# Performance work log

Measured on AMD Instinct MI355X. Metric: run time of the kernel, lower is better.

The kernel has to match this reference:

```python
import jax, jax.numpy as jnp
import numpy as np
import math

D_MODEL = 1024
D_STATE = 16
D_CONV = 4
EXPAND = 2
NHEADS = 8
NGROUPS = 1
D_INNER = D_MODEL * EXPAND                      # 2048
D_SSM = D_INNER - 2 * NGROUPS * D_STATE          # 2016
HEADP = D_SSM // NHEADS                          # 252
D_IN_PROJ = 4 * D_INNER + NHEADS                 # 8200
BATCH = 2
SEQLEN = 2048
DT_MIN, DT_MAX, DT_FLOOR = 1e-3, 1e-1, 1e-4


def setup_inputs() -> dict:
    key = jax.random.key(0)
    ks = jax.random.split(key, 10)
    rn = lambda k, shape, scale: (jax.random.normal(k, shape, jnp.float32) * scale)
    # dt_bias init exactly like the torch module
    dt = jnp.exp(jax.random.uniform(ks[0], (NHEADS,)) * (math.log(DT_MAX) - math.log(DT_MIN)) + math.log(DT_MIN))
    dt = jnp.clip(dt, DT_FLOOR, None)
    dt_bias = dt + jnp.log(-jnp.expm1(-dt))
    A_log = jnp.log(jax.random.uniform(ks[1], (NHEADS,), minval=0.9, maxval=0.999))
    return {
        "u": rn(ks[2], (BATCH, SEQLEN, D_MODEL), 1.0),
        "W_in": rn(ks[3], (D_MODEL, D_IN_PROJ), 0.02),
        "conv_w": rn(ks[4], (D_INNER, D_CONV), 0.2),
        "conv_b": rn(ks[5], (D_INNER,), 0.02),
        "dt_bias": dt_bias,
        "A_log": A_log,
        "Dp": jnp.ones((NHEADS,), jnp.float32),
        "ln_g": jnp.ones((D_SSM,), jnp.float32),
        "ln_b": jnp.zeros((D_SSM,), jnp.float32),
        "gate_w": rn(ks[6], (D_SSM, D_SSM), 0.02),
        "gate_b": jnp.zeros((D_SSM,), jnp.float32),
        "W_out": rn(ks[7], (D_INNER + D_SSM, D_MODEL), 0.02),
    }


def _forward(u, W_in, conv_w, conv_b, dt_bias, A_log, Dp, ln_g, ln_b, gate_w, gate_b, W_out):
    B, L, _ = u.shape
    zxbcdt = jnp.einsum('bld,de->ble', u, W_in)  # [B,L,4*Di+H]
    z0 = zxbcdt[..., :D_INNER]
    x0 = zxbcdt[..., D_INNER:2 * D_INNER]
    # z (2*Di:3*Di) is unused in the original forward
    xBC = zxbcdt[..., 3 * D_INNER:4 * D_INNER]
    dt_raw = zxbcdt[..., 4 * D_INNER:]              # [B,L,H]
    dt = jax.nn.softplus(dt_raw + dt_bias)           # [B,L,H]
    A = -jnp.exp(A_log)                              # [H]
    # depthwise causal conv1d (kernel D_CONV) + SiLU
    xc = jnp.pad(xBC, ((0, 0), (D_CONV - 1, 0), (0, 0)))
    xBC_conv = conv_b + sum(xc[:, k:k + L, :] * conv_w[:, k] for k in range(D_CONV))
    xBC_act = jax.nn.silu(xBC_conv)                  # [B,L,Di]
    x = xBC_act[..., :D_SSM].reshape(B, L, NHEADS, HEADP)   # [B,L,H,P]
    Bm = xBC_act[..., D_SSM:D_SSM + D_STATE]         # [B,L,N] (ngroups=1)
    Cm = xBC_act[..., D_SSM + D_STATE:]              # [B,L,N]

    def step(h, inp):
        dt_t, x_t, B_t, C_t = inp                    # [b,H],[b,H,P],[b,N],[b,N]
        dA = jnp.exp(dt_t * A)                       # [b,H]
        h = dA[:, :, None, None] * h + (dt_t[:, :, None] * x_t)[..., None] * B_t[:, None, None, :]
        y_t = jnp.einsum('bhpn,bn->bhp', h, C_t) + Dp[None, :, None] * x_t
        return h, y_t

    h0 = jnp.zeros((B, NHEADS, HEADP, D_STATE), u.dtype)
    xs = (dt.transpose(1, 0, 2), x.transpose(1, 0, 2, 3), Bm.transpose(1, 0, 2), Cm.transpose(1, 0, 2))
    _, ys = jax.lax.scan(step, h0, xs)               # ys: [L,B,H,P]
    y = ys.transpose(1, 0, 2, 3).reshape(B, L, D_SSM)
    # LayerNorm over d_ssm
    mu = y.mean(-1, keepdims=True)
    var = y.var(-1, keepdims=True)
    y = (y - mu) * jax.lax.rsqrt(var + 1e-5) * ln_g + ln_b
    gate = jax.nn.sigmoid(jnp.einsum('bld,de->ble', y, gate_w) + gate_b)
    y = gate * y
    mlp_skip = jax.nn.silu(z0) * x0                  # [B,L,Di]
    return jnp.einsum('ble,ed->bld', jnp.concatenate([mlp_skip, y], axis=-1), W_out)


def reference(u, W_in, conv_w, conv_b, dt_bias, A_log, Dp, ln_g, ln_b, gate_w, gate_b, W_out):
    return _forward(u, W_in, conv_w, conv_b, dt_bias, A_log, Dp, ln_g, ln_b, gate_w, gate_b, W_out)
```

## Files before the change

### kernel.cpp

```cpp
#include <hip/hip_runtime.h>
#include <hip/hip_bf16.h>
#include <math.h>

#define ROWS   4096
#define SEQLEN 2048
#define DMODEL 1024
#define DINNER 2048
#define DSSM   2016
#define NHEADS 8
#define HEADP  252
#define NPROJ  6152
#define LDPROJ 8200
#define NCAT   4064
#define NC     16
#define LC     128
#define STATE  4032

typedef unsigned short u16;
typedef __attribute__((ext_vector_type(8))) short bf16x8;
typedef __attribute__((ext_vector_type(4))) float f32x4;

__device__ __forceinline__ float sigmoidf_(float x){ return 1.f/(1.f+__expf(-x)); }
__device__ __forceinline__ float siluf_(float x){ return x/(1.f+__expf(-x)); }
__device__ __forceinline__ u16 f2b(float f){ __hip_bfloat16 h = __float2bfloat16(f); return *reinterpret_cast<u16*>(&h); }
__device__ __forceinline__ float b2f(u16 s){ __hip_bfloat16 h; *reinterpret_cast<u16*>(&h)=s; return __bfloat162float(h); }

__device__ __forceinline__ void gload16(const u16* g, u16* l) {
  __builtin_amdgcn_global_load_lds(
      (const __attribute__((address_space(1))) void*)g,
      (__attribute__((address_space(3))) void*)l, 16, 0, 0);
}

__global__ __launch_bounds__(256)
void cvt_k(const float* __restrict__ in, u16* __restrict__ out, int n4)
{
  int i = blockIdx.x*256 + threadIdx.x;
  if (i >= n4) return;
  float4 v = ((const float4*)in)[i];
  ushort4 o; o.x=f2b(v.x); o.y=f2b(v.y); o.z=f2b(v.z); o.w=f2b(v.w);
  ((ushort4*)out)[i] = o;
}

template<int REMAP>
__global__ __launch_bounds__(256)
void transcvt_k(const float* __restrict__ W, u16* __restrict__ Wt,
                int K, int N, int ldw)
{
  __shared__ float t[32][33];
  const int n0 = blockIdx.x*32, k0 = blockIdx.y*32;
  const int li = threadIdx.x & 31, lj = threadIdx.x >> 5;
  #pragma unroll
  for (int r = 0; r < 4; r++) {
    int k = k0 + lj + r*8, n = n0 + li;
    float v = 0.f;
    if (n < N) {
      int ns = REMAP ? (n < 4096 ? n : n + 2048) : n;
      v = W[(size_t)k*ldw + ns];
    }
    t[lj + r*8][li] = v;
  }
  __syncthreads();
  #pragma unroll
  for (int r = 0; r < 4; r++) {
    int n = n0 + lj + r*8, k = k0 + li;
    Wt[(size_t)n*K + k] = f2b(t[li][lj + r*8]);
  }
}

template<int MODE>
__global__ __launch_bounds__(256)
void mgemm_k(const u16* __restrict__ A, const u16* __restrict__ Bt,
             float* __restrict__ Cf, u16* __restrict__ Cb,
             const float* __restrict__ bias,
             int M, int N, int K, int ldc)
{
  __shared__ __align__(16) u16 As[128*32];
  __shared__ __align__(16) u16 Bs[128*32];
  const int tid = threadIdx.x;
  const int lane = tid & 63, wid = tid >> 6;
  const int wr = wid >> 1, wc = wid & 1;
  const int row0 = blockIdx.y * 128, col0 = blockIdx.x * 128;
  const int lg = lane >> 4, lr = lane & 15;

  const u16* gA = A  + (size_t)(row0 + wid*32 + (lane>>2))*K + (lane&3)*8;
  const u16* gB = Bt + (size_t)(col0 + wid*32 + (lane>>2))*K + (lane&3)*8;
  u16* lA = &As[wid*32*32];
  u16* lB = &Bs[wid*32*32];

  f32x4 acc[4][4];
  #pragma unroll
  for (int m=0;m<4;m++)
    #pragma unroll
    for (int n=0;n<4;n++) acc[m][n] = (f32x4){0.f,0.f,0.f,0.f};

  for (int k0 = 0; k0 < K; k0 += 32) {
    __syncthreads();
    gload16(gA,                lA);
    gload16(gA + (size_t)16*K, lA + 16*32);
    gload16(gB,                lB);
    gload16(gB + (size_t)16*K, lB + 16*32);
    gA += 32; gB += 32;
    __syncthreads();

    bf16x8 af[4], bfr[4];
    #pragma unroll
    for (int m=0;m<4;m++) af[m]  = *(const bf16x8*)&As[(wr*64 + m*16 + lr)*32 + lg*8];
    #pragma unroll
    for (int n=0;n<4;n++) bfr[n] = *(const bf16x8*)&Bs[(wc*64 + n*16 + lr)*32 + lg*8];
    #pragma unroll
    for (int m=0;m<4;m++)
      #pragma unroll
      for (int n=0;n<4;n++)
        acc[m][n] = __builtin_amdgcn_mfma_f32_16x16x32_bf16(af[m], bfr[n], acc[m][n], 0, 0, 0);
  }

  #pragma unroll
  for (int m=0;m<4;m++) {
    #pragma unroll
    for (int n=0;n<4;n++) {
      int colb = col0 + wc*64 + n*16 + lr;
      if (colb >= N) continue;
      #pragma unroll
      for (int r=0;r<4;r++) {
        int row = row0 + wr*64 + m*16 + lg*4 + r;
        float v = acc[m][n][r];
        if (MODE == 1) {
          v = sigmoidf_(v + bias[colb]) * b2f(A[(size_t)row*K + colb]);
          Cb[(size_t)row*NCAT + 2048 + colb] = f2b(v);
        } else {
          Cf[(size_t)row*ldc + colb] = v;
        }
      }
    }
  }
}

__global__ __launch_bounds__(256)
void dt_k(const float* __restrict__ zx, const float* __restrict__ dt_bias,
          float* __restrict__ dtb)
{
  int idx = blockIdx.x*256 + threadIdx.x;
  int r = idx >> 3, hh = idx & 7;
  float v = zx[(size_t)r*NPROJ + 6144 + hh] + dt_bias[hh];
  dtb[idx] = (v > 20.f) ? v : log1pf(__expf(v));
}

__global__ __launch_bounds__(256)
void conv_silu_k(const float* __restrict__ zx, const float* __restrict__ cw,
                 const float* __restrict__ cb, float* __restrict__ actb)
{
  int idx = blockIdx.x*256 + threadIdx.x;
  int c = idx & (DINNER-1);
  int r = idx >> 11;
  int l = r & (SEQLEN-1);
  float s = cb[c];
  #pragma unroll
  for (int k = 0; k < 4; k++) {
    int ll = l - 3 + k;
    if (ll >= 0) s += zx[(size_t)(r-3+k)*NPROJ + 4096 + c] * cw[c*4 + k];
  }
  actb[idx] = siluf_(s);
}

__global__ __launch_bounds__(256)
void mlp_k(const float* __restrict__ zx, u16* __restrict__ cat)
{
  int idx = blockIdx.x*256 + threadIdx.x;
  int j = idx & (DINNER-1);
  int r = idx >> 11;
  float z = zx[(size_t)r*NPROJ + j];
  float x = zx[(size_t)r*NPROJ + 2048 + j];
  cat[(size_t)r*NCAT + j] = f2b(siluf_(z) * x);
}

#define CH 32
__global__ __launch_bounds__(256)
void scan1_k(const float* __restrict__ actb, const float* __restrict__ dtb,
             const float* __restrict__ A_log,
             float* __restrict__ hloc, float* __restrict__ Pbuf)
{
  const int blk = blockIdx.x;
  const int c = blk & (NC-1), bh = blk >> 4;
  const int hh = bh & 7, b = bh >> 3;
  const int tid = threadIdx.x;
  const float Ah = -__expf(A_log[hh]);
  float h[16];
  #pragma unroll
  for (int n = 0; n < 16; n++) h[n] = 0.f;
  float dtsum = 0.f;

  __shared__ float xs[CH][HEADP+4];
  __shared__ float bs[CH][16];
  __shared__ float dts[CH];
  const int rowbase = b*SEQLEN + c*LC;

  for (int c0 = 0; c0 < LC; c0 += CH) {
    __syncthreads();
    #pragma unroll 4
    for (int s = 0; s < CH; s++) {
      const size_t rr = (size_t)(rowbase + c0 + s) * DINNER;
      if (tid < HEADP) xs[s][tid] = actb[rr + hh*HEADP + tid];
      if (tid >= 224 && tid < 240) bs[s][tid-224] = actb[rr + DSSM + (tid-224)];
    }
    if (tid < CH) dts[tid] = dtb[(size_t)(rowbase + c0 + tid)*NHEADS + hh];
    __syncthreads();

    for (int s = 0; s < CH; s++) {
      float dtv = dts[s];
      float dA  = __expf(dtv * Ah);
      float xv  = (tid < HEADP) ? xs[s][tid] : 0.f;
      float w   = dtv * xv;
      const float4* Bp = (const float4*)&bs[s][0];
      #pragma unroll
      for (int q = 0; q < 4; q++) {
        float4 Bv = Bp[q];
        h[4*q+0] = dA*h[4*q+0] + w*Bv.x;
        h[4*q+1] = dA*h[4*q+1] + w*Bv.y;
        h[4*q+2] = dA*h[4*q+2] + w*Bv.z;
        h[4*q+3] = dA*h[4*q+3] + w*Bv.w;
      }
      dtsum += dts[s];
    }
  }
  if (tid < HEADP) {
    float4* dst = (float4*)&hloc[((size_t)bh*NC + c)*STATE + tid*16];
    dst[0] = make_float4(h[0],h[1],h[2],h[3]);
    dst[1] = make_float4(h[4],h[5],h[6],h[7]);
    dst[2] = make_float4(h[8],h[9],h[10],h[11]);
    dst[3] = make_float4(h[12],h[13],h[14],h[15]);
  }
  if (tid == 0) Pbuf[bh*NC + c] = __expf(Ah * dtsum);
}

__global__ __launch_bounds__(256)
void comb_k(const float* __restrict__ hloc, const float* __restrict__ Pbuf,
            float* __restrict__ Hinit)
{
  const int bh = blockIdx.x;
  const int tid = threadIdx.x;
  __shared__ float Ps[NC];
  if (tid < NC) Ps[tid] = Pbuf[bh*NC + tid];
  __syncthreads();
  for (int e = tid; e < STATE; e += 256) {
    float H = 0.f;
    const float* hl = &hloc[(size_t)bh*NC*STATE + e];
    float* Hi = &Hinit[(size_t)bh*NC*STATE + e];
    #pragma unroll
    for (int cc = 0; cc < NC; cc++) {
      Hi[(size_t)cc*STATE] = H;
      H = Ps[cc]*H + hl[(size_t)cc*STATE];
    }
  }
}

__global__ __launch_bounds__(256)
void scan2_k(const float* __restrict__ actb, const float* __restrict__ dtb,
             const float* __restrict__ A_log, const float* __restrict__ Dp,
             const float* __restrict__ Hinit, float* __restrict__ y)
{
  const int blk = blockIdx.x;
  const int c = blk & (NC-1), bh = blk >> 4;
  const int hh = bh & 7, b = bh >> 3;
  const int tid = threadIdx.x;
  const float Ah = -__expf(A_log[hh]);
  const float Dv = Dp[hh];
  float h[16];
  if (tid < HEADP) {
    const float4* src = (const float4*)&Hinit[((size_t)bh*NC + c)*STATE + tid*16];
    float4 a0=src[0], a1=src[1], a2=src[2], a3=src[3];
    h[0]=a0.x; h[1]=a0.y; h[2]=a0.z; h[3]=a0.w;
    h[4]=a1.x; h[5]=a1.y; h[6]=a1.z; h[7]=a1.w;
    h[8]=a2.x; h[9]=a2.y; h[10]=a2.z; h[11]=a2.w;
    h[12]=a3.x; h[13]=a3.y; h[14]=a3.z; h[15]=a3.w;
  } else {
    #pragma unroll
    for (int n = 0; n < 16; n++) h[n] = 0.f;
  }

  __shared__ float xs[CH][HEADP+4];
  __shared__ float bcs[CH][32];
  __shared__ float dts[CH];
  const int rowbase = b*SEQLEN + c*LC;

  for (int c0 = 0; c0 < LC; c0 += CH) {
    __syncthreads();
    #pragma unroll 4
    for (int s = 0; s < CH; s++) {
      const size_t rr = (size_t)(rowbase + c0 + s) * DINNER;
      if (tid < HEADP) xs[s][tid] = actb[rr + hh*HEADP + tid];
      if (tid >= 224)  bcs[s][tid-224] = actb[rr + DSSM + (tid-224)];
    }
    if (tid < CH) dts[tid] = dtb[(size_t)(rowbase + c0 + tid)*NHEADS + hh];
    __syncthreads();

    for (int s = 0; s < CH; s++) {
      float dtv = dts[s];
      float dA  = __expf(dtv * Ah);
      float xv  = (tid < HEADP) ? xs[s][tid] : 0.f;
      float w   = dtv * xv;
      float acc = Dv * xv;
      const float4* Bp = (const float4*)&bcs[s][0];
      const float4* Cp = (const float4*)&bcs[s][16];
      #pragma unroll
      for (int q = 0; q < 4; q++) {
        float4 Bv = Bp[q], Cv = Cp[q];
        h[4*q+0] = dA*h[4*q+0] + w*Bv.x; acc += h[4*q+0]*Cv.x;
        h[4*q+1] = dA*h[4*q+1] + w*Bv.y; acc += h[4*q+1]*Cv.y;
        h[4*q+2] = dA*h[4*q+2] + w*Bv.z; acc += h[4*q+2]*Cv.z;
        h[4*q+3] = dA*h[4*q+3] + w*Bv.w; acc += h[4*q+3]*Cv.w;
      }
      if (tid < HEADP)
        y[(size_t)(rowbase + c0 + s)*DSSM + hh*HEADP + tid] = acc;
    }
  }
}

__global__ __launch_bounds__(256)
void ln_k(const float* __restrict__ y, const float* __restrict__ g,
          const float* __restrict__ bta, u16* __restrict__ yb)
{
  const int r = blockIdx.x;
  const int tid = threadIdx.x;
  __shared__ float r1[4], r2[4];
  __shared__ float smu, srs;
  float s1 = 0.f, s2 = 0.f;
  for (int i = tid; i < DSSM; i += 256) {
    float v = y[(size_t)r*DSSM + i];
    s1 += v; s2 += v*v;
  }
  #pragma unroll
  for (int o = 32; o > 0; o >>= 1) { s1 += __shfl_down(s1, o, 64); s2 += __shfl_down(s2, o, 64); }
  if ((tid & 63) == 0) { r1[tid>>6] = s1; r2[tid>>6] = s2; }
  __syncthreads();
  if (tid == 0) {
    float a1 = r1[0]+r1[1]+r1[2]+r1[3];
    float a2 = r2[0]+r2[1]+r2[2]+r2[3];
    float mu = a1 / (float)DSSM;
    float var = a2 / (float)DSSM - mu*mu;
    smu = mu; srs = rsqrtf(var + 1e-5f);
  }
  __syncthreads();
  float mu = smu, rs = srs;
  for (int i = tid; i < DSSM; i += 256) {
    float v = (y[(size_t)r*DSSM + i] - mu) * rs * g[i] + bta[i];
    yb[(size_t)r*DSSM + i] = f2b(v);
  }
}

extern "C" void kernel_launch(void* const* d_in, const int* in_sizes, int n_in,
                              void* d_out, int out_size, void* d_ws, size_t ws_size,
                              hipStream_t stream)
{
  const float* u      = (const float*)d_in[0];
  const float* W_in   = (const float*)d_in[1];
  const float* conv_w = (const float*)d_in[2];
  const float* conv_b = (const float*)d_in[3];
  const float* dt_bias= (const float*)d_in[4];
  const float* A_log  = (const float*)d_in[5];
  const float* Dp     = (const float*)d_in[6];
  const float* ln_g   = (const float*)d_in[7];
  const float* ln_b   = (const float*)d_in[8];
  const float* gate_w = (const float*)d_in[9];
  const float* gate_b = (const float*)d_in[10];
  const float* W_out  = (const float*)d_in[11];
  float* out = (float*)d_out;

  float* ws   = (float*)d_ws;
  float* zx   = ws;
  float* actb = zx   + (size_t)ROWS*NPROJ;
  float* dtb  = actb + (size_t)ROWS*DINNER;
  u16* u_bf   = (u16*)(dtb + (size_t)ROWS*NHEADS);
  u16* Wint   = u_bf  + (size_t)ROWS*DMODEL;
  u16* yb_bf  = Wint  + (size_t)6272*DMODEL;
  u16* cat_bf = yb_bf + (size_t)ROWS*DSSM;
  float* yb    = zx;
  float* hloc  = zx + (size_t)ROWS*DSSM;
  float* Hinit = hloc + (size_t)16*NC*STATE;
  float* Pbuf  = Hinit + (size_t)16*NC*STATE;
  u16* gwt    = (u16*)actb;
  u16* wot    = gwt + (size_t)2048*DSSM;

  dim3 blk(256);
  cvt_k<<<dim3((ROWS*DMODEL/4 + 255)/256), blk, 0, stream>>>(u, u_bf, ROWS*DMODEL/4);
  transcvt_k<1><<<dim3(6272/32, DMODEL/32), blk, 0, stream>>>(W_in, Wint, DMODEL, NPROJ, LDPROJ);
  mgemm_k<0><<<dim3(49, 32), blk, 0, stream>>>(u_bf, Wint, zx, nullptr, nullptr,
                                               ROWS, NPROJ, DMODEL, NPROJ);
  dt_k<<<dim3(ROWS*NHEADS/256), blk, 0, stream>>>(zx, dt_bias, dtb);
  conv_silu_k<<<dim3(ROWS*DINNER/256), blk, 0, stream>>>(zx, conv_w, conv_b, actb);
  mlp_k<<<dim3(ROWS*DINNER/256), blk, 0, stream>>>(zx, cat_bf);
  scan1_k<<<dim3(16*NC), blk, 0, stream>>>(actb, dtb, A_log, hloc, Pbuf);
  comb_k<<<dim3(16), blk, 0, stream>>>(hloc, Pbuf, Hinit);
  scan2_k<<<dim3(16*NC), blk, 0, stream>>>(actb, dtb, A_log, Dp, Hinit, yb);
  ln_k<<<dim3(ROWS), blk, 0, stream>>>(yb, ln_g, ln_b, yb_bf);
  transcvt_k<0><<<dim3(2048/32, DSSM/32), blk, 0, stream>>>(gate_w, gwt, DSSM, DSSM, DSSM);
  mgemm_k<1><<<dim3(16, 32), blk, 0, stream>>>(yb_bf, gwt, nullptr, cat_bf, gate_b,
                                               ROWS, DSSM, DSSM, 0);
  transcvt_k<0><<<dim3(1024/32, NCAT/32), blk, 0, stream>>>(W_out, wot, NCAT, DMODEL, DMODEL);
  mgemm_k<2><<<dim3(8, 32), blk, 0, stream>>>(cat_bf, wot, out, nullptr, nullptr,
                                              ROWS, DMODEL, NCAT, DMODEL);
}
```

Baseline: 705.0 us.

## Double-buffer GEMM LDS tiles and split scan into more, shorter chunks

The bf16 MFMA GEMM now keeps two LDS buffers per operand. It issues the global-to-LDS loads for the next K-tile before computing the current one, with one barrier per iteration instead of two, so memory latency can overlap with MFMA work. Separately, the chunked selective scan goes from 16 chunks of 128 steps to 64 chunks of 32 steps. This gives scan1/scan2 four times as many blocks for parallelism. The cost is a longer sequential combine pass in comb_k and four times the chunk-state memory traffic, plus doubled LDS use in the GEMM, which may reduce occupancy.

```diff
diff --git a/kernel.cpp b/kernel.cpp
--- a/kernel.cpp
+++ b/kernel.cpp
@@ -12,8 +12,8 @@
 #define NPROJ  6152
 #define LDPROJ 8200
 #define NCAT   4064
-#define NC     16
-#define LC     128
+#define NC     64
+#define LC     32
 #define STATE  4032
 
 typedef unsigned short u16;
@@ -74,8 +74,8 @@
              const float* __restrict__ bias,
              int M, int N, int K, int ldc)
 {
-  __shared__ __align__(16) u16 As[128*32];
-  __shared__ __align__(16) u16 Bs[128*32];
+  __shared__ __align__(16) u16 As[2][128*32];
+  __shared__ __align__(16) u16 Bs[2][128*32];
   const int tid = threadIdx.x;
   const int lane = tid & 63, wid = tid >> 6;
   const int wr = wid >> 1, wc = wid & 1;
@@ -84,8 +84,7 @@
 
   const u16* gA = A  + (size_t)(row0 + wid*32 + (lane>>2))*K + (lane&3)*8;
   const u16* gB = Bt + (size_t)(col0 + wid*32 + (lane>>2))*K + (lane&3)*8;
-  u16* lA = &As[wid*32*32];
-  u16* lB = &Bs[wid*32*32];
+  const int lofs = wid*32*32;
 
   f32x4 acc[4][4];
   #pragma unroll
@@ -93,26 +92,37 @@
     #pragma unroll
     for (int n=0;n<4;n++) acc[m][n] = (f32x4){0.f,0.f,0.f,0.f};
 
-  for (int k0 = 0; k0 < K; k0 += 32) {
-    __syncthreads();
-    gload16(gA,                lA);
-    gload16(gA + (size_t)16*K, lA + 16*32);
-    gload16(gB,                lB);
-    gload16(gB + (size_t)16*K, lB + 16*32);
+  auto stage = [&](int buf) {
+    gload16(gA,                &As[buf][lofs]);
+    gload16(gA + (size_t)16*K, &As[buf][lofs + 16*32]);
+    gload16(gB,                &Bs[buf][lofs]);
+    gload16(gB + (size_t)16*K, &Bs[buf][lofs + 16*32]);
     gA += 32; gB += 32;
-    __syncthreads();
-
+  };
+  auto compute = [&](int buf) {
     bf16x8 af[4], bfr[4];
     #pragma unroll
-    for (int m=0;m<4;m++) af[m]  = *(const bf16x8*)&As[(wr*64 + m*16 + lr)*32 + lg*8];
-    #pragma unroll
-    for (int n=0;n<4;n++) bfr[n] = *(const bf16x8*)&Bs[(wc*64 + n*16 + lr)*32 + lg*8];
+    for (int m=0;m<4;m++) af[m]  = *(const bf16x8*)&As[buf][(wr*64 + m*16 + lr)*32 + lg*8];
+    #pragma unroll
+    for (int n=0;n<4;n++) bfr[n] = *(const bf16x8*)&Bs[buf][(wc*64 + n*16 + lr)*32 + lg*8];
     #pragma unroll
     for (int m=0;m<4;m++)
       #pragma unroll
       for (int n=0;n<4;n++)
         acc[m][n] = __builtin_amdgcn_mfma_f32_16x16x32_bf16(af[m], bfr[n], acc[m][n], 0, 0, 0);
-  }
+  };
+
+  const int nt = K >> 5;
+  stage(0);
+  __syncthreads();
+  int cur = 0;
+  for (int t = 1; t < nt; ++t) {
+    stage(cur ^ 1);
+    compute(cur);
+    __syncthreads();
+    cur ^= 1;
+  }
+  compute(cur);
 
   #pragma unroll
   for (int m=0;m<4;m++) {
@@ -180,7 +190,7 @@
              float* __restrict__ hloc, float* __restrict__ Pbuf)
 {
   const int blk = blockIdx.x;
-  const int c = blk & (NC-1), bh = blk >> 4;
+  const int c = blk & (NC-1), bh = blk >> 6;
   const int hh = bh & 7, b = bh >> 3;
   const int tid = threadIdx.x;
   const float Ah = -__expf(A_log[hh]);
@@ -239,13 +249,12 @@
   const int bh = blockIdx.x;
   const int tid = threadIdx.x;
   __shared__ float Ps[NC];
-  if (tid < NC) Ps[tid] = Pbuf[bh*NC + tid];
+  for (int i = tid; i < NC; i += 256) Ps[i] = Pbuf[bh*NC + i];
   __syncthreads();
   for (int e = tid; e < STATE; e += 256) {
     float H = 0.f;
     const float* hl = &hloc[(size_t)bh*NC*STATE + e];
     float* Hi = &Hinit[(size_t)bh*NC*STATE + e];
-    #pragma unroll
     for (int cc = 0; cc < NC; cc++) {
       Hi[(size_t)cc*STATE] = H;
       H = Ps[cc]*H + hl[(size_t)cc*STATE];
@@ -259,7 +268,7 @@
              const float* __restrict__ Hinit, float* __restrict__ y)
 {
   const int blk = blockIdx.x;
-  const int c = blk & (NC-1), bh = blk >> 4;
+  const int c = blk & (NC-1), bh = blk >> 6;
   const int hh = bh & 7, b = bh >> 3;
   const int tid = threadIdx.x;
   const float Ah = -__expf(A_log[hh]);
```

Result: slower. 777.9 us (+10.3%).
